# Kernel tuning notes

Hardware: AMD Instinct MI355X
Metric: run time of the kernel (lower is better)

## Reference

```python
import jax, jax.numpy as jnp
import numpy as np

B, N1, N2, E = 128, 128, 384, 1024
N = N1 + N2
D_IN, D_FC = 64, 128
NUM_HEADS = 8.0  # args.num_att_heads
THETA = 1.0      # args.al_scale


def setup_inputs() -> dict:
    key = jax.random.key(0)
    ks = jax.random.split(key, 14)
    c_hs = jax.random.normal(ks[0], (B, N, D_IN), jnp.float32)
    attention = jax.random.uniform(ks[1], (B, N1, N2), jnp.float32)
    coords = jax.random.normal(ks[2], (B, N, 3), jnp.float32)
    upd_coords = coords + 0.1 * jax.random.normal(ks[3], (B, N, 3), jnp.float32)
    c_valid = jnp.ones((B, N), jnp.float32)
    nm = (jax.random.uniform(ks[4], (B, N1)) < 0.7).astype(jnp.float32)
    mapping = (jax.random.uniform(ks[5], (B, N, N)) < 0.05).astype(jnp.float32)
    samelb = jnp.maximum(mapping, (jax.random.uniform(ks[6], (B, N, N)) < 0.1).astype(jnp.float32))
    edge_index = jax.random.randint(ks[7], (B, E, 2), 0, N1, jnp.int32)
    W0 = jax.random.normal(ks[8], (D_IN, D_FC), jnp.float32) * 0.05
    b0 = jnp.zeros((D_FC,), jnp.float32)
    W1 = jax.random.normal(ks[9], (D_FC, D_FC), jnp.float32) * 0.05
    b1 = jnp.zeros((D_FC,), jnp.float32)
    W2 = jax.random.normal(ks[10], (D_FC, D_FC), jnp.float32) * 0.05
    b2 = jnp.zeros((D_FC,), jnp.float32)
    W3 = jax.random.normal(ks[11], (D_FC, 1), jnp.float32) * 0.05
    b3 = jnp.zeros((1,), jnp.float32)
    return dict(c_hs=c_hs, attention=attention, coords=coords, upd_coords=upd_coords,
                c_valid=c_valid, nm=nm, mapping=mapping, samelb=samelb,
                edge_index=edge_index, W0=W0, b0=b0, W1=W1, b1=b1, W2=W2, b2=b2, W3=W3, b3=b3)


def _kabsch(P, Q, m):
    # P, Q: [N1, 3], m: [N1] 0/1 non-modified mask
    Pm = P.mean(0)
    Qm = Q.mean(0)
    h = (P - Pm).T @ (Q - Qm) / NUM_HEADS  # [3,3]
    u, s, vt = jnp.linalg.svd(h)
    d = jnp.sign(jnp.linalg.det(h))
    corr = jnp.diag(jnp.concatenate([jnp.ones((2,), h.dtype), d[None].astype(h.dtype)]))
    r = u @ corr @ vt
    trans = Qm - r @ Pm
    Pp = P @ r.T + trans
    mk = (m > 0.5).astype(P.dtype)[:, None]
    cnt = jnp.maximum(mk.sum() * 3.0, 1.0)
    new_rmsd = (mk * (Pp - Q) ** 2).sum() / cnt        # mse over selected rows
    cen = ((Pp.mean(0) - Qm) ** 2).mean()              # centroid mse
    return new_rmsd, cen


def reference(c_hs, attention, coords, upd_coords, c_valid, nm, mapping, samelb,
              edge_index, W0, b0, W1, b1, W2, b2, W3, b3):
    # --- segment-sum pooling (sum_var_parts) + divide by n1, then FC head ---
    pooled = (c_hs * c_valid[..., None]).sum(axis=1) / float(N1)   # [B, D_IN]
    h = jax.nn.relu(pooled @ W0 + b0)
    h = jax.nn.relu(h @ W1 + b1)
    h = jax.nn.relu(h @ W2 + b2)
    scores = jax.nn.sigmoid(h @ W3 + b3).reshape(-1)               # [B]

    # --- cal_atten_batch + F.normalize(dim=1) ---
    atten = jnp.zeros((B, N, N), c_hs.dtype)
    atten = atten.at[:, :N1, N1:].set(attention)
    atten = atten.at[:, N1:, :N1].set(jnp.swapaxes(attention, 1, 2))
    nrm = jnp.sqrt((atten ** 2).sum(axis=1, keepdims=True))
    atten = atten / jnp.maximum(nrm, 1e-12)

    # --- cal_attn_loss ---
    top = jnp.where(mapping == 1.0, jnp.exp(-(atten * mapping)), 0.0).sum(axis=(1, 2))
    topabot = jnp.where(samelb == 1.0, jnp.exp(-(atten * samelb)), 0.0).sum(axis=(1, 2))
    attn_loss = (top / (topabot - top + 1.0)).sum() * THETA / float(B)

    # --- cal_rmsd_loss: straight-through one-hot mapping + Kabsch/SVD ---
    PP = upd_coords[:, :N1]   # subgraph updated coords
    QQ = coords[:, N1:]       # target graph original coords
    oh = jax.nn.one_hot(jnp.argmax(attention, axis=-1), N2, dtype=attention.dtype)
    st = oh + attention - jax.lax.stop_gradient(attention)         # straight-through
    Qsel = jnp.einsum('bij,bjd->bid', st, QQ)                      # [B, N1, 3]
    new_rmsd, cen = jax.vmap(_kabsch)(PP, Qsel, nm)
    rmsd_loss = new_rmsd.mean()
    centroid_loss = cen.mean()

    # --- cal_pairdst_loss over subgraph edges ---
    sub_c = coords[:, :N1]
    sub_u = upd_coords[:, :N1]
    bidx = jnp.arange(B)[:, None]
    d0 = jnp.sqrt(((sub_c[bidx, edge_index[..., 0]] - sub_c[bidx, edge_index[..., 1]]) ** 2).sum(-1) + 1e-12)
    d1 = jnp.sqrt(((sub_u[bidx, edge_index[..., 0]] - sub_u[bidx, edge_index[..., 1]]) ** 2).sum(-1) + 1e-12)
    pairdst_loss = jnp.abs((d1 - d0).sum(axis=-1)).mean()

    return scores, attn_loss, rmsd_loss, pairdst_loss, centroid_loss
```

## Files before the change

### kernel.cpp

```cpp
#include <hip/hip_runtime.h>
#include <math.h>

#define B_   128
#define N1_  128
#define N2_  384
#define N_   512
#define E_   1024
#define DIN  64
#define DFC  128

#define ACC_TOP  0
#define ACC_BOT  128
#define POOL_OFF 256
#define RNI_OFF  (POOL_OFF + B_*DIN)
#define CNI_OFF  (RNI_OFF + B_*N1_)
#define BI_OFF   (CNI_OFF + B_*N2_)
#define EB_OFF   (BI_OFF + B_*N1_)
#define ZERO_CNT (POOL_OFF + B_*DIN)

__global__ void k_init(float* ws, float* out) {
    int idx = blockIdx.x * 256 + threadIdx.x;
    if (idx < ZERO_CNT) ws[idx] = 0.f;
    if (blockIdx.x == 0 && threadIdx.x < 4) out[128 + threadIdx.x] = 0.f;
}

__global__ void k_pool(const float* __restrict__ c_hs, const float* __restrict__ c_valid,
                       float* __restrict__ ws) {
    __shared__ float4 sred[256];
    int b = blockIdx.x, t = threadIdx.x;
    int chunk = blockIdx.y * 64;
    int d4 = t & 15, rl = t >> 4;
    const float4* X4 = (const float4*)(c_hs + (size_t)b * N_ * DIN);
    const float* V = c_valid + (size_t)b * N_;
    float4 acc = {0.f, 0.f, 0.f, 0.f};
    #pragma unroll
    for (int r = chunk + rl; r < chunk + 64; r += 16) {
        float4 x = X4[r * 16 + d4];
        float v = V[r];
        acc.x += x.x * v; acc.y += x.y * v; acc.z += x.z * v; acc.w += x.w * v;
    }
    sred[t] = acc; __syncthreads();
    for (int off = 128; off >= 16; off >>= 1) {
        if (t < off) {
            float4 o = sred[t + off];
            sred[t].x += o.x; sred[t].y += o.y; sred[t].z += o.z; sred[t].w += o.w;
        }
        __syncthreads();
    }
    if (t < 16) {
        float4 s = sred[t];
        float* p = ws + POOL_OFF + b * DIN + t * 4;
        atomicAdd(&p[0], s.x); atomicAdd(&p[1], s.y);
        atomicAdd(&p[2], s.z); atomicAdd(&p[3], s.w);
    }
}

__global__ void k_mlp2(const float* __restrict__ ws,
                       const float* __restrict__ W0, const float* __restrict__ b0,
                       const float* __restrict__ W1, const float* __restrict__ b1,
                       const float* __restrict__ W2, const float* __restrict__ b2,
                       const float* __restrict__ W3, const float* __restrict__ b3,
                       float* __restrict__ out) {
    __shared__ float pool[DIN];
    __shared__ float h[DFC];
    __shared__ float h2[DFC];
    __shared__ float part[DFC];
    int b = blockIdx.x, t = threadIdx.x;
    if (t < DIN) pool[t] = ws[POOL_OFF + b * DIN + t] * (1.0f / 128.0f);
    __syncthreads();
    float a = b0[t];
    #pragma unroll
    for (int i = 0; i < DIN; ++i) a += pool[i] * W0[i * DFC + t];
    h[t] = fmaxf(a, 0.f); __syncthreads();
    a = b1[t];
    #pragma unroll
    for (int i = 0; i < DFC; ++i) a += h[i] * W1[i * DFC + t];
    h2[t] = fmaxf(a, 0.f); __syncthreads();
    a = b2[t];
    #pragma unroll
    for (int i = 0; i < DFC; ++i) a += h2[i] * W2[i * DFC + t];
    part[t] = fmaxf(a, 0.f) * W3[t];
    __syncthreads();
    for (int off = 64; off > 0; off >>= 1) { if (t < off) part[t] += part[t + off]; __syncthreads(); }
    if (t == 0) out[b] = 1.f / (1.f + expf(-(part[0] + b3[0])));
}

__global__ void k_rows(const float* __restrict__ att, float* __restrict__ ws) {
    int b = blockIdx.x, t = threadIdx.x, wv = t >> 6, ln = t & 63;
    int r = blockIdx.y * 4 + wv;
    const float* row = att + ((size_t)b * N1_ + r) * N2_;
    float ssq = 0.f, best = -1e30f; int bidx = 0;
    #pragma unroll
    for (int q = 0; q < 6; ++q) {
        float v = row[ln + 64 * q];
        ssq += v * v;
        if (v > best) { best = v; bidx = ln + 64 * q; }
    }
    for (int off = 32; off > 0; off >>= 1) {
        ssq += __shfl_xor(ssq, off, 64);
        float ov = __shfl_xor(best, off, 64);
        int oi = __shfl_xor(bidx, off, 64);
        if (ov > best || (ov == best && oi < bidx)) { best = ov; bidx = oi; }
    }
    if (ln == 0) {
        ws[RNI_OFF + b * N1_ + r] = 1.f / fmaxf(sqrtf(ssq), 1e-12f);
        ((int*)ws)[BI_OFF + b * N1_ + r] = bidx;
    }
}

__global__ void k_cols(const float* __restrict__ att, float* __restrict__ ws) {
    __shared__ float sred[256];
    int b = blockIdx.x, t = threadIdx.x;
    int c = blockIdx.y * 64 + (t & 63);
    int q = t >> 6;
    const float* A = att + (size_t)b * N1_ * N2_;
    float s = 0.f;
    #pragma unroll 8
    for (int j = q * 32; j < q * 32 + 32; ++j) { float v = A[j * N2_ + c]; s += v * v; }
    sred[t] = s; __syncthreads();
    if (t < 64)
        ws[CNI_OFF + b * N2_ + blockIdx.y * 64 + t] =
            1.f / fmaxf(sqrtf(sred[t] + sred[t + 64] + sred[t + 128] + sred[t + 192]), 1e-12f);
}

#define TP 129
__global__ void k_prep(const float* __restrict__ att, float* __restrict__ ws) {
    __shared__ float tile[32 * TP];
    __shared__ float rinv[N1_];
    int b = blockIdx.y, t = threadIdx.x;
    int r0 = blockIdx.x * 32;
    if (t < N1_) rinv[t] = ws[RNI_OFF + b * N1_ + t];
    __syncthreads();
    const float4* att4 = (const float4*)(att + (size_t)b * N1_ * N2_);
    int c8 = t & 7, jb = t >> 3;
    #pragma unroll
    for (int p = 0; p < 4; ++p) {
        int j = jb + p * 32;
        float4 a = att4[j * 96 + blockIdx.x * 8 + c8];
        float rv = rinv[j];
        tile[(c8 * 4 + 0) * TP + j] = a.x * rv;
        tile[(c8 * 4 + 1) * TP + j] = a.y * rv;
        tile[(c8 * 4 + 2) * TP + j] = a.z * rv;
        tile[(c8 * 4 + 3) * TP + j] = a.w * rv;
    }
    __syncthreads();
    int j4 = t & 31, cb = t >> 5;
    float4* eb4 = (float4*)(ws + EB_OFF + ((size_t)b * N2_ + r0) * N1_);
    #pragma unroll
    for (int p = 0; p < 4; ++p) {
        int c = cb + p * 8;
        float4 e;
        e.x = __expf(-tile[c * TP + j4 * 4]);
        e.y = __expf(-tile[c * TP + j4 * 4 + 1]);
        e.z = __expf(-tile[c * TP + j4 * 4 + 2]);
        e.w = __expf(-tile[c * TP + j4 * 4 + 3]);
        eb4[c * 32 + j4] = e;
    }
}

__device__ inline float cnt4(float4 m) {
    return (m.x == 1.f ? 1.f : 0.f) + (m.y == 1.f ? 1.f : 0.f)
         + (m.z == 1.f ? 1.f : 0.f) + (m.w == 1.f ? 1.f : 0.f);
}

__global__ void k_scan(const float* __restrict__ att, const float* __restrict__ mapping,
                       const float* __restrict__ samelb, float* __restrict__ ws) {
    __shared__ float cninv[N2_];
    __shared__ float rt[4], rb[4];
    int b = blockIdx.y, t = threadIdx.x;
    int i0 = blockIdx.x * 16;
    const float4* m4 = (const float4*)(mapping + ((size_t)b * N_ + i0) * N_);
    const float4* s4 = (const float4*)(samelb + ((size_t)b * N_ + i0) * N_);
    float top = 0.f, bot = 0.f;
    if (i0 < N1_) {
        for (int j = t; j < N2_; j += 256) cninv[j] = ws[CNI_OFF + b * N2_ + j];
        __syncthreads();
        #pragma unroll
        for (int k = 0; k < 2; ++k) {
            int g = t + k * 256; int r = g >> 5, c4 = g & 31;
            top += cnt4(m4[r * 128 + c4]);
            bot += cnt4(s4[r * 128 + c4]);
        }
        const float4* a4 = (const float4*)(att + ((size_t)b * N1_ + i0) * N2_);
        #pragma unroll
        for (int k = 0; k < 6; ++k) {
            int g = t + k * 256; int r = g / 96, c4 = g - r * 96;
            float4 mv = m4[r * 128 + 32 + c4];
            float4 sv = s4[r * 128 + 32 + c4];
            float4 a  = a4[r * 96 + c4];
            int cb = c4 * 4;
            float e0 = __expf(-a.x * cninv[cb]);
            float e1 = __expf(-a.y * cninv[cb + 1]);
            float e2 = __expf(-a.z * cninv[cb + 2]);
            float e3 = __expf(-a.w * cninv[cb + 3]);
            top += (mv.x == 1.f ? e0 : 0.f) + (mv.y == 1.f ? e1 : 0.f)
                 + (mv.z == 1.f ? e2 : 0.f) + (mv.w == 1.f ? e3 : 0.f);
            bot += (sv.x == 1.f ? e0 : 0.f) + (sv.y == 1.f ? e1 : 0.f)
                 + (sv.z == 1.f ? e2 : 0.f) + (sv.w == 1.f ? e3 : 0.f);
        }
    } else {
        const float4* eb4 = (const float4*)(ws + EB_OFF + ((size_t)b * N2_ + (i0 - N1_)) * N1_);
        #pragma unroll
        for (int k = 0; k < 2; ++k) {
            int g = t + k * 256; int r = g >> 5, c4 = g & 31;
            float4 mv = m4[r * 128 + c4];
            float4 sv = s4[r * 128 + c4];
            float4 e  = eb4[r * 32 + c4];
            top += (mv.x == 1.f ? e.x : 0.f) + (mv.y == 1.f ? e.y : 0.f)
                 + (mv.z == 1.f ? e.z : 0.f) + (mv.w == 1.f ? e.w : 0.f);
            bot += (sv.x == 1.f ? e.x : 0.f) + (sv.y == 1.f ? e.y : 0.f)
                 + (sv.z == 1.f ? e.z : 0.f) + (sv.w == 1.f ? e.w : 0.f);
        }
        #pragma unroll
        for (int k = 0; k < 6; ++k) {
            int g = t + k * 256; int r = g / 96, c4 = g - r * 96;
            top += cnt4(m4[r * 128 + 32 + c4]);
            bot += cnt4(s4[r * 128 + 32 + c4]);
        }
    }
    for (int off = 32; off > 0; off >>= 1) {
        top += __shfl_down(top, off, 64);
        bot += __shfl_down(bot, off, 64);
    }
    int wv = t >> 6, ln = t & 63;
    if (ln == 0) { rt[wv] = top; rb[wv] = bot; }
    __syncthreads();
    if (t == 0) {
        atomicAdd(&ws[ACC_TOP + b], rt[0] + rt[1] + rt[2] + rt[3]);
        atomicAdd(&ws[ACC_BOT + b], rb[0] + rb[1] + rb[2] + rb[3]);
    }
}

__device__ inline float bred(float* s2, float v, int t) {
    for (int off = 32; off > 0; off >>= 1) v += __shfl_down(v, off, 64);
    if ((t & 63) == 0) s2[t >> 6] = v;
    __syncthreads();
    float r = s2[0] + s2[1];
    __syncthreads();
    return r;
}

__global__ void k_kabsch(const float* __restrict__ coords, const float* __restrict__ upd,
                         const float* __restrict__ nm, const int* __restrict__ ei,
                         const float* __restrict__ ws, float* __restrict__ out) {
    __shared__ float s2[2];
    __shared__ float Rsh[9], Tsh[3];
    int b = blockIdx.x, t = threadIdx.x;
    int bidx = ((const int*)ws)[BI_OFF + b * N1_ + t];
    float P[3], Q[3];
    const float* up = upd + ((size_t)b * N_ + t) * 3;
    P[0] = up[0]; P[1] = up[1]; P[2] = up[2];
    const float* qp = coords + ((size_t)b * N_ + N1_ + bidx) * 3;
    Q[0] = qp[0]; Q[1] = qp[1]; Q[2] = qp[2];
    float Pm[3], Qm[3];
    for (int a = 0; a < 3; ++a) Pm[a] = bred(s2, P[a], t) * (1.f / 128.f);
    for (int a = 0; a < 3; ++a) Qm[a] = bred(s2, Q[a], t) * (1.f / 128.f);
    float H[9];
    for (int a = 0; a < 3; ++a)
        for (int c = 0; c < 3; ++c)
            H[a * 3 + c] = bred(s2, (P[a] - Pm[a]) * (Q[c] - Qm[c]), t) * (1.f / 8.f);
    if (t == 0) {
        double Hd[3][3];
        for (int a = 0; a < 3; ++a) for (int c = 0; c < 3; ++c) Hd[a][c] = (double)H[a * 3 + c];
        double A[3][3], V[3][3] = {{1,0,0},{0,1,0},{0,0,1}};
        for (int i = 0; i < 3; ++i)
            for (int j = 0; j < 3; ++j) {
                double z = 0; for (int c = 0; c < 3; ++c) z += Hd[c][i] * Hd[c][j];
                A[i][j] = z;
            }
        for (int sweep = 0; sweep < 8; ++sweep) {
            const int PQ[3][2] = {{0,1},{0,2},{1,2}};
            for (int r = 0; r < 3; ++r) {
                int p = PQ[r][0], q = PQ[r][1];
                double apq = A[p][q];
                if (fabs(apq) < 1e-300) continue;
                double tau = (A[q][q] - A[p][p]) / (2.0 * apq);
                double tt = (tau >= 0 ? 1.0 : -1.0) / (fabs(tau) + sqrt(1.0 + tau * tau));
                double c = 1.0 / sqrt(1.0 + tt * tt), s = tt * c;
                for (int k = 0; k < 3; ++k) { double akp = A[k][p], akq = A[k][q]; A[k][p] = c * akp - s * akq; A[k][q] = s * akp + c * akq; }
                for (int k = 0; k < 3; ++k) { double apk = A[p][k], aqk = A[q][k]; A[p][k] = c * apk - s * aqk; A[q][k] = s * apk + c * aqk; }
                for (int k = 0; k < 3; ++k) { double vkp = V[k][p], vkq = V[k][q]; V[k][p] = c * vkp - s * vkq; V[k][q] = s * vkp + c * vkq; }
            }
        }
        double lam[3] = {A[0][0], A[1][1], A[2][2]};
        int id[3] = {0, 1, 2};
        if (lam[id[0]] < lam[id[1]]) { int x = id[0]; id[0] = id[1]; id[1] = x; }
        if (lam[id[0]] < lam[id[2]]) { int x = id[0]; id[0] = id[2]; id[2] = x; }
        if (lam[id[1]] < lam[id[2]]) { int x = id[1]; id[1] = id[2]; id[2] = x; }
        double u[3][3], v[3][3], sv[3];
        for (int i = 0; i < 3; ++i) {
            for (int k = 0; k < 3; ++k) v[i][k] = V[k][id[i]];
            double uv[3];
            for (int c = 0; c < 3; ++c) uv[c] = Hd[c][0] * v[i][0] + Hd[c][1] * v[i][1] + Hd[c][2] * v[i][2];
            double n = sqrt(uv[0] * uv[0] + uv[1] * uv[1] + uv[2] * uv[2]);
            sv[i] = n;
            if (n > 1e-150) { u[i][0] = uv[0] / n; u[i][1] = uv[1] / n; u[i][2] = uv[2] / n; }
            else { u[i][0] = u[i][1] = u[i][2] = 0.0; }
        }
        if (sv[2] < 1e-12 * fmax(sv[0], 1e-300)) {
            u[2][0] = u[0][1] * u[1][2] - u[0][2] * u[1][1];
            u[2][1] = u[0][2] * u[1][0] - u[0][0] * u[1][2];
            u[2][2] = u[0][0] * u[1][1] - u[0][1] * u[1][0];
        }
        double det = Hd[0][0] * (Hd[1][1] * Hd[2][2] - Hd[1][2] * Hd[2][1])
                   - Hd[0][1] * (Hd[1][0] * Hd[2][2] - Hd[1][2] * Hd[2][0])
                   + Hd[0][2] * (Hd[1][0] * Hd[2][1] - Hd[1][1] * Hd[2][0]);
        double dsg = (det > 0.0) ? 1.0 : ((det < 0.0) ? -1.0 : 0.0);
        for (int a = 0; a < 3; ++a)
            for (int c = 0; c < 3; ++c)
                Rsh[a * 3 + c] = (float)(u[0][a] * v[0][c] + u[1][a] * v[1][c] + dsg * u[2][a] * v[2][c]);
        for (int a = 0; a < 3; ++a)
            Tsh[a] = Qm[a] - (Rsh[a * 3] * Pm[0] + Rsh[a * 3 + 1] * Pm[1] + Rsh[a * 3 + 2] * Pm[2]);
    }
    __syncthreads();
    float Pp[3];
    for (int a = 0; a < 3; ++a)
        Pp[a] = Rsh[a * 3] * P[0] + Rsh[a * 3 + 1] * P[1] + Rsh[a * 3 + 2] * P[2] + Tsh[a];
    float mk = (nm[b * N1_ + t] > 0.5f) ? 1.f : 0.f;
    float dx = Pp[0] - Q[0], dy = Pp[1] - Q[1], dz = Pp[2] - Q[2];
    float rsum = bred(s2, mk * (dx * dx + dy * dy + dz * dz), t);
    float msum = bred(s2, mk, t);
    float Ppm[3];
    for (int a = 0; a < 3; ++a) Ppm[a] = bred(s2, Pp[a], t) * (1.f / 128.f);
    if (t == 0) {
        float cnt = fmaxf(msum * 3.f, 1.f);
        atomicAdd(&out[129], (rsum / cnt) * (1.f / 128.f));
        float cen = 0.f;
        for (int a = 0; a < 3; ++a) { float d2 = Ppm[a] - Qm[a]; cen += d2 * d2; }
        atomicAdd(&out[131], (cen / 3.f) * (1.f / 128.f));
    }
    const float* C = coords + (size_t)b * N_ * 3;
    const float* U = upd + (size_t)b * N_ * 3;
    const int* e = ei + (size_t)b * E_ * 2;
    float acc = 0.f;
    for (int idx = t; idx < E_; idx += 128) {
        int a0 = e[idx * 2], a1 = e[idx * 2 + 1];
        float ex = C[a0 * 3] - C[a1 * 3], ey = C[a0 * 3 + 1] - C[a1 * 3 + 1], ez = C[a0 * 3 + 2] - C[a1 * 3 + 2];
        float d0 = sqrtf(ex * ex + ey * ey + ez * ez + 1e-12f);
        ex = U[a0 * 3] - U[a1 * 3]; ey = U[a0 * 3 + 1] - U[a1 * 3 + 1]; ez = U[a0 * 3 + 2] - U[a1 * 3 + 2];
        float d1 = sqrtf(ex * ex + ey * ey + ez * ez + 1e-12f);
        acc += d1 - d0;
    }
    float psum = bred(s2, acc, t);
    if (t == 0) atomicAdd(&out[130], fabsf(psum) * (1.f / 128.f));
    if (b == 0) {
        float top = ws[ACC_TOP + t], bot = ws[ACC_BOT + t];
        float v = top / (bot - top + 1.0f);
        float s = bred(s2, v, t);
        if (t == 0) out[128] = s * (1.0f / 128.0f);
    }
}

extern "C" void kernel_launch(void* const* d_in, const int* in_sizes, int n_in,
                              void* d_out, int out_size, void* d_ws, size_t ws_size,
                              hipStream_t stream) {
    const float* c_hs      = (const float*)d_in[0];
    const float* attention = (const float*)d_in[1];
    const float* coords    = (const float*)d_in[2];
    const float* upd       = (const float*)d_in[3];
    const float* c_valid   = (const float*)d_in[4];
    const float* nm        = (const float*)d_in[5];
    const float* mapping   = (const float*)d_in[6];
    const float* samelb    = (const float*)d_in[7];
    const int*   ei        = (const int*)d_in[8];
    const float* W0 = (const float*)d_in[9],  *b0 = (const float*)d_in[10];
    const float* W1 = (const float*)d_in[11], *b1 = (const float*)d_in[12];
    const float* W2 = (const float*)d_in[13], *b2 = (const float*)d_in[14];
    const float* W3 = (const float*)d_in[15], *b3 = (const float*)d_in[16];
    float* out = (float*)d_out;
    float* ws  = (float*)d_ws;

    hipLaunchKernelGGL(k_init,   dim3(33),      dim3(256), 0, stream, ws, out);
    hipLaunchKernelGGL(k_pool,   dim3(B_, 8),   dim3(256), 0, stream, c_hs, c_valid, ws);
    hipLaunchKernelGGL(k_mlp2,   dim3(B_),      dim3(DFC), 0, stream, ws,
                       W0, b0, W1, b1, W2, b2, W3, b3, out);
    hipLaunchKernelGGL(k_rows,   dim3(B_, 32),  dim3(256), 0, stream, attention, ws);
    hipLaunchKernelGGL(k_cols,   dim3(B_, 6),   dim3(256), 0, stream, attention, ws);
    hipLaunchKernelGGL(k_prep,   dim3(12, B_),  dim3(256), 0, stream, attention, ws);
    hipLaunchKernelGGL(k_scan,   dim3(32, B_),  dim3(256), 0, stream, attention, mapping, samelb, ws);
    hipLaunchKernelGGL(k_kabsch, dim3(B_),      dim3(N1_), 0, stream, coords, upd, nm, ei, ws, out);
}
```

Before: 389.9 us.

## Precompute attention exponentials and stage scan tiles into LDS via direct global loads

```diff
diff --git a/kernel.cpp b/kernel.cpp
--- a/kernel.cpp
+++ b/kernel.cpp
@@ -16,7 +16,14 @@
 #define CNI_OFF  (RNI_OFF + B_*N1_)
 #define BI_OFF   (CNI_OFF + B_*N2_)
 #define EB_OFF   (BI_OFF + B_*N1_)
+#define EA_OFF   (EB_OFF + B_*N1_*N2_)
 #define ZERO_CNT (POOL_OFF + B_*DIN)
+
+__device__ __forceinline__ void ld_lds16(const float* g, float* l) {
+    __builtin_amdgcn_global_load_lds(
+        (const __attribute__((address_space(1))) void*)g,
+        (__attribute__((address_space(3))) void*)l, 16, 0, 0);
+}
 
 __global__ void k_init(float* ws, float* out) {
     int idx = blockIdx.x * 256 + threadIdx.x;
@@ -123,6 +130,28 @@
             1.f / fmaxf(sqrtf(sred[t] + sred[t + 64] + sred[t + 128] + sred[t + 192]), 1e-12f);
 }
 
+__global__ void k_prepA(const float* __restrict__ att, float* __restrict__ ws) {
+    __shared__ float cni[N2_];
+    int b = blockIdx.x, t = threadIdx.x;
+    int r0 = blockIdx.y * 16;
+    for (int j = t; j < N2_; j += 256) cni[j] = ws[CNI_OFF + b * N2_ + j];
+    __syncthreads();
+    const float4* a4 = (const float4*)(att + ((size_t)b * N1_ + r0) * N2_);
+    float4* e4 = (float4*)(ws + EA_OFF + ((size_t)b * N1_ + r0) * N2_);
+    #pragma unroll
+    for (int k = 0; k < 6; ++k) {
+        int idx = t + k * 256;
+        int c4 = idx % 96; int cb = c4 * 4;
+        float4 a = a4[idx];
+        float4 e;
+        e.x = __expf(-a.x * cni[cb]);
+        e.y = __expf(-a.y * cni[cb + 1]);
+        e.z = __expf(-a.z * cni[cb + 2]);
+        e.w = __expf(-a.w * cni[cb + 3]);
+        e4[idx] = e;
+    }
+}
+
 #define TP 129
 __global__ void k_prep(const float* __restrict__ att, float* __restrict__ ws) {
     __shared__ float tile[32 * TP];
@@ -158,71 +187,59 @@
     }
 }
 
-__device__ inline float cnt4(float4 m) {
-    return (m.x == 1.f ? 1.f : 0.f) + (m.y == 1.f ? 1.f : 0.f)
-         + (m.z == 1.f ? 1.f : 0.f) + (m.w == 1.f ? 1.f : 0.f);
-}
-
-__global__ void k_scan(const float* __restrict__ att, const float* __restrict__ mapping,
-                       const float* __restrict__ samelb, float* __restrict__ ws) {
-    __shared__ float cninv[N2_];
+__global__ void k_scan(const float* __restrict__ mapping, const float* __restrict__ samelb,
+                       float* __restrict__ ws) {
+    __shared__ float4 lm4[512];
+    __shared__ float4 ls4[512];
+    __shared__ float4 le4[384];
     __shared__ float rt[4], rb[4];
     int b = blockIdx.y, t = threadIdx.x;
-    int i0 = blockIdx.x * 16;
-    const float4* m4 = (const float4*)(mapping + ((size_t)b * N_ + i0) * N_);
-    const float4* s4 = (const float4*)(samelb + ((size_t)b * N_ + i0) * N_);
+    int i0 = blockIdx.x * 4;
+    int wv = t >> 6, ln = t & 63;
+    float* lm = (float*)lm4;
+    float* lsm = (float*)ls4;
+    const float* gm = mapping + ((size_t)b * N_ + i0) * N_;
+    const float* gs = samelb + ((size_t)b * N_ + i0) * N_;
+    for (int g = wv; g < 8; g += 4) ld_lds16(gm + g * 256 + ln * 4, lm + g * 256);
+    for (int g = wv; g < 8; g += 4) ld_lds16(gs + g * 256 + ln * 4, lsm + g * 256);
+    bool typeA = (i0 < N1_);
+    if (typeA) {
+        const float* ge = ws + EA_OFF + ((size_t)b * N1_ + i0) * N2_;
+        for (int g = wv; g < 6; g += 4) ld_lds16(ge + g * 256 + ln * 4, (float*)le4 + g * 256);
+    } else {
+        const float* ge = ws + EB_OFF + ((size_t)b * N2_ + (i0 - N1_)) * N1_;
+        for (int g = wv; g < 2; g += 4) ld_lds16(ge + g * 256 + ln * 4, (float*)le4 + g * 256);
+    }
+    __syncthreads();
+    const float4 ONES = {1.f, 1.f, 1.f, 1.f};
     float top = 0.f, bot = 0.f;
-    if (i0 < N1_) {
-        for (int j = t; j < N2_; j += 256) cninv[j] = ws[CNI_OFF + b * N2_ + j];
-        __syncthreads();
+    if (typeA) {
         #pragma unroll
         for (int k = 0; k < 2; ++k) {
-            int g = t + k * 256; int r = g >> 5, c4 = g & 31;
-            top += cnt4(m4[r * 128 + c4]);
-            bot += cnt4(s4[r * 128 + c4]);
-        }
-        const float4* a4 = (const float4*)(att + ((size_t)b * N1_ + i0) * N2_);
-        #pragma unroll
-        for (int k = 0; k < 6; ++k) {
-            int g = t + k * 256; int r = g / 96, c4 = g - r * 96;
-            float4 mv = m4[r * 128 + 32 + c4];
-            float4 sv = s4[r * 128 + 32 + c4];
-            float4 a  = a4[r * 96 + c4];
-            int cb = c4 * 4;
-            float e0 = __expf(-a.x * cninv[cb]);
-            float e1 = __expf(-a.y * cninv[cb + 1]);
-            float e2 = __expf(-a.z * cninv[cb + 2]);
-            float e3 = __expf(-a.w * cninv[cb + 3]);
-            top += (mv.x == 1.f ? e0 : 0.f) + (mv.y == 1.f ? e1 : 0.f)
-                 + (mv.z == 1.f ? e2 : 0.f) + (mv.w == 1.f ? e3 : 0.f);
-            bot += (sv.x == 1.f ? e0 : 0.f) + (sv.y == 1.f ? e1 : 0.f)
-                 + (sv.z == 1.f ? e2 : 0.f) + (sv.w == 1.f ? e3 : 0.f);
+            int idx = t + k * 256;
+            int row = idx >> 7, c4 = idx & 127;
+            float4 m = lm4[idx], s = ls4[idx];
+            int ei = row * 96 + ((c4 < 32) ? 0 : (c4 - 32));
+            float4 w = (c4 < 32) ? ONES : le4[ei];
+            top += m.x * w.x + m.y * w.y + m.z * w.z + m.w * w.w;
+            bot += s.x * w.x + s.y * w.y + s.z * w.z + s.w * w.w;
         }
     } else {
-        const float4* eb4 = (const float4*)(ws + EB_OFF + ((size_t)b * N2_ + (i0 - N1_)) * N1_);
         #pragma unroll
         for (int k = 0; k < 2; ++k) {
-            int g = t + k * 256; int r = g >> 5, c4 = g & 31;
-            float4 mv = m4[r * 128 + c4];
-            float4 sv = s4[r * 128 + c4];
-            float4 e  = eb4[r * 32 + c4];
-            top += (mv.x == 1.f ? e.x : 0.f) + (mv.y == 1.f ? e.y : 0.f)
-                 + (mv.z == 1.f ? e.z : 0.f) + (mv.w == 1.f ? e.w : 0.f);
-            bot += (sv.x == 1.f ? e.x : 0.f) + (sv.y == 1.f ? e.y : 0.f)
-                 + (sv.z == 1.f ? e.z : 0.f) + (sv.w == 1.f ? e.w : 0.f);
-        }
-        #pragma unroll
-        for (int k = 0; k < 6; ++k) {
-            int g = t + k * 256; int r = g / 96, c4 = g - r * 96;
-            top += cnt4(m4[r * 128 + 32 + c4]);
-            bot += cnt4(s4[r * 128 + 32 + c4]);
+            int idx = t + k * 256;
+            int row = idx >> 7, c4 = idx & 127;
+            float4 m = lm4[idx], s = ls4[idx];
+            int ei = row * 32 + ((c4 < 32) ? c4 : 0);
+            float4 w = (c4 < 32) ? le4[ei] : ONES;
+            top += m.x * w.x + m.y * w.y + m.z * w.z + m.w * w.w;
+            bot += s.x * w.x + s.y * w.y + s.z * w.z + s.w * w.w;
         }
     }
     for (int off = 32; off > 0; off >>= 1) {
         top += __shfl_down(top, off, 64);
         bot += __shfl_down(bot, off, 64);
     }
-    int wv = t >> 6, ln = t & 63;
     if (ln == 0) { rt[wv] = top; rb[wv] = bot; }
     __syncthreads();
     if (t == 0) {
@@ -376,7 +393,8 @@
                        W0, b0, W1, b1, W2, b2, W3, b3, out);
     hipLaunchKernelGGL(k_rows,   dim3(B_, 32),  dim3(256), 0, stream, attention, ws);
     hipLaunchKernelGGL(k_cols,   dim3(B_, 6),   dim3(256), 0, stream, attention, ws);
+    hipLaunchKernelGGL(k_prepA,  dim3(B_, 8),   dim3(256), 0, stream, attention, ws);
     hipLaunchKernelGGL(k_prep,   dim3(12, B_),  dim3(256), 0, stream, attention, ws);
-    hipLaunchKernelGGL(k_scan,   dim3(32, B_),  dim3(256), 0, stream, attention, mapping, samelb, ws);
+    hipLaunchKernelGGL(k_scan,   dim3(128, B_), dim3(256), 0, stream, mapping, samelb, ws);
     hipLaunchKernelGGL(k_kabsch, dim3(B_),      dim3(N1_), 0, stream, coords, upd, nm, ei, ws, out);
 }
```

New measurement: 410.1 us. 1.05x slower.

## Merge front-end kernels, fold MLP into Kabsch launch, and simplify scan to two rows per block

Applied to the files above, without the earlier changes.

```diff
diff --git a/kernel.cpp b/kernel.cpp
--- a/kernel.cpp
+++ b/kernel.cpp
@@ -24,103 +24,70 @@
     if (blockIdx.x == 0 && threadIdx.x < 4) out[128 + threadIdx.x] = 0.f;
 }
 
-__global__ void k_pool(const float* __restrict__ c_hs, const float* __restrict__ c_valid,
-                       float* __restrict__ ws) {
-    __shared__ float4 sred[256];
-    int b = blockIdx.x, t = threadIdx.x;
-    int chunk = blockIdx.y * 64;
-    int d4 = t & 15, rl = t >> 4;
-    const float4* X4 = (const float4*)(c_hs + (size_t)b * N_ * DIN);
-    const float* V = c_valid + (size_t)b * N_;
-    float4 acc = {0.f, 0.f, 0.f, 0.f};
-    #pragma unroll
-    for (int r = chunk + rl; r < chunk + 64; r += 16) {
-        float4 x = X4[r * 16 + d4];
-        float v = V[r];
-        acc.x += x.x * v; acc.y += x.y * v; acc.z += x.z * v; acc.w += x.w * v;
-    }
-    sred[t] = acc; __syncthreads();
-    for (int off = 128; off >= 16; off >>= 1) {
-        if (t < off) {
-            float4 o = sred[t + off];
-            sred[t].x += o.x; sred[t].y += o.y; sred[t].z += o.z; sred[t].w += o.w;
-        }
-        __syncthreads();
-    }
-    if (t < 16) {
-        float4 s = sred[t];
-        float* p = ws + POOL_OFF + b * DIN + t * 4;
-        atomicAdd(&p[0], s.x); atomicAdd(&p[1], s.y);
-        atomicAdd(&p[2], s.z); atomicAdd(&p[3], s.w);
-    }
-}
-
-__global__ void k_mlp2(const float* __restrict__ ws,
-                       const float* __restrict__ W0, const float* __restrict__ b0,
-                       const float* __restrict__ W1, const float* __restrict__ b1,
-                       const float* __restrict__ W2, const float* __restrict__ b2,
-                       const float* __restrict__ W3, const float* __restrict__ b3,
-                       float* __restrict__ out) {
-    __shared__ float pool[DIN];
-    __shared__ float h[DFC];
-    __shared__ float h2[DFC];
-    __shared__ float part[DFC];
-    int b = blockIdx.x, t = threadIdx.x;
-    if (t < DIN) pool[t] = ws[POOL_OFF + b * DIN + t] * (1.0f / 128.0f);
-    __syncthreads();
-    float a = b0[t];
-    #pragma unroll
-    for (int i = 0; i < DIN; ++i) a += pool[i] * W0[i * DFC + t];
-    h[t] = fmaxf(a, 0.f); __syncthreads();
-    a = b1[t];
-    #pragma unroll
-    for (int i = 0; i < DFC; ++i) a += h[i] * W1[i * DFC + t];
-    h2[t] = fmaxf(a, 0.f); __syncthreads();
-    a = b2[t];
-    #pragma unroll
-    for (int i = 0; i < DFC; ++i) a += h2[i] * W2[i * DFC + t];
-    part[t] = fmaxf(a, 0.f) * W3[t];
-    __syncthreads();
-    for (int off = 64; off > 0; off >>= 1) { if (t < off) part[t] += part[t + off]; __syncthreads(); }
-    if (t == 0) out[b] = 1.f / (1.f + expf(-(part[0] + b3[0])));
-}
-
-__global__ void k_rows(const float* __restrict__ att, float* __restrict__ ws) {
-    int b = blockIdx.x, t = threadIdx.x, wv = t >> 6, ln = t & 63;
-    int r = blockIdx.y * 4 + wv;
-    const float* row = att + ((size_t)b * N1_ + r) * N2_;
-    float ssq = 0.f, best = -1e30f; int bidx = 0;
-    #pragma unroll
-    for (int q = 0; q < 6; ++q) {
-        float v = row[ln + 64 * q];
-        ssq += v * v;
-        if (v > best) { best = v; bidx = ln + 64 * q; }
-    }
-    for (int off = 32; off > 0; off >>= 1) {
-        ssq += __shfl_xor(ssq, off, 64);
-        float ov = __shfl_xor(best, off, 64);
-        int oi = __shfl_xor(bidx, off, 64);
-        if (ov > best || (ov == best && oi < bidx)) { best = ov; bidx = oi; }
-    }
-    if (ln == 0) {
-        ws[RNI_OFF + b * N1_ + r] = 1.f / fmaxf(sqrtf(ssq), 1e-12f);
-        ((int*)ws)[BI_OFF + b * N1_ + r] = bidx;
-    }
-}
-
-__global__ void k_cols(const float* __restrict__ att, float* __restrict__ ws) {
-    __shared__ float sred[256];
-    int b = blockIdx.x, t = threadIdx.x;
-    int c = blockIdx.y * 64 + (t & 63);
-    int q = t >> 6;
-    const float* A = att + (size_t)b * N1_ * N2_;
-    float s = 0.f;
-    #pragma unroll 8
-    for (int j = q * 32; j < q * 32 + 32; ++j) { float v = A[j * N2_ + c]; s += v * v; }
-    sred[t] = s; __syncthreads();
-    if (t < 64)
-        ws[CNI_OFF + b * N2_ + blockIdx.y * 64 + t] =
-            1.f / fmaxf(sqrtf(sred[t] + sred[t + 64] + sred[t + 128] + sred[t + 192]), 1e-12f);
+__global__ void k_front(const float* __restrict__ c_hs, const float* __restrict__ c_valid,
+                        const float* __restrict__ att, float* __restrict__ ws) {
+    __shared__ float4 sred4[256];
+    float* sred = (float*)sred4;
+    int b = blockIdx.x, y = blockIdx.y, t = threadIdx.x;
+    if (y < 8) {
+        int chunk = y * 64;
+        int d4 = t & 15, rl = t >> 4;
+        const float4* X4 = (const float4*)(c_hs + (size_t)b * N_ * DIN);
+        const float* V = c_valid + (size_t)b * N_;
+        float4 acc = {0.f, 0.f, 0.f, 0.f};
+        #pragma unroll
+        for (int r = chunk + rl; r < chunk + 64; r += 16) {
+            float4 x = X4[r * 16 + d4];
+            float v = V[r];
+            acc.x += x.x * v; acc.y += x.y * v; acc.z += x.z * v; acc.w += x.w * v;
+        }
+        sred4[t] = acc; __syncthreads();
+        for (int off = 128; off >= 16; off >>= 1) {
+            if (t < off) {
+                float4 o = sred4[t + off];
+                sred4[t].x += o.x; sred4[t].y += o.y; sred4[t].z += o.z; sred4[t].w += o.w;
+            }
+            __syncthreads();
+        }
+        if (t < 16) {
+            float4 s = sred4[t];
+            float* p = ws + POOL_OFF + b * DIN + t * 4;
+            atomicAdd(&p[0], s.x); atomicAdd(&p[1], s.y);
+            atomicAdd(&p[2], s.z); atomicAdd(&p[3], s.w);
+        }
+    } else if (y < 40) {
+        int wv = t >> 6, ln = t & 63;
+        int r = (y - 8) * 4 + wv;
+        const float* row = att + ((size_t)b * N1_ + r) * N2_;
+        float ssq = 0.f, best = -1e30f; int bidx = 0;
+        #pragma unroll
+        for (int q = 0; q < 6; ++q) {
+            float v = row[ln + 64 * q];
+            ssq += v * v;
+            if (v > best) { best = v; bidx = ln + 64 * q; }
+        }
+        for (int off = 32; off > 0; off >>= 1) {
+            ssq += __shfl_xor(ssq, off, 64);
+            float ov = __shfl_xor(best, off, 64);
+            int oi = __shfl_xor(bidx, off, 64);
+            if (ov > best || (ov == best && oi < bidx)) { best = ov; bidx = oi; }
+        }
+        if (ln == 0) {
+            ws[RNI_OFF + b * N1_ + r] = 1.f / fmaxf(sqrtf(ssq), 1e-12f);
+            ((int*)ws)[BI_OFF + b * N1_ + r] = bidx;
+        }
+    } else {
+        int c = (y - 40) * 64 + (t & 63);
+        int q = t >> 6;
+        const float* A = att + (size_t)b * N1_ * N2_;
+        float s = 0.f;
+        #pragma unroll 8
+        for (int j = q * 32; j < q * 32 + 32; ++j) { float v = A[j * N2_ + c]; s += v * v; }
+        sred[t] = s; __syncthreads();
+        if (t < 64)
+            ws[CNI_OFF + b * N2_ + (y - 40) * 64 + t] =
+                1.f / fmaxf(sqrtf(sred[t] + sred[t + 64] + sred[t + 128] + sred[t + 192]), 1e-12f);
+    }
 }
 
 #define TP 129
@@ -158,66 +125,34 @@
     }
 }
 
-__device__ inline float cnt4(float4 m) {
-    return (m.x == 1.f ? 1.f : 0.f) + (m.y == 1.f ? 1.f : 0.f)
-         + (m.z == 1.f ? 1.f : 0.f) + (m.w == 1.f ? 1.f : 0.f);
-}
-
 __global__ void k_scan(const float* __restrict__ att, const float* __restrict__ mapping,
                        const float* __restrict__ samelb, float* __restrict__ ws) {
-    __shared__ float cninv[N2_];
     __shared__ float rt[4], rb[4];
     int b = blockIdx.y, t = threadIdx.x;
-    int i0 = blockIdx.x * 16;
-    const float4* m4 = (const float4*)(mapping + ((size_t)b * N_ + i0) * N_);
-    const float4* s4 = (const float4*)(samelb + ((size_t)b * N_ + i0) * N_);
-    float top = 0.f, bot = 0.f;
-    if (i0 < N1_) {
-        for (int j = t; j < N2_; j += 256) cninv[j] = ws[CNI_OFF + b * N2_ + j];
-        __syncthreads();
-        #pragma unroll
-        for (int k = 0; k < 2; ++k) {
-            int g = t + k * 256; int r = g >> 5, c4 = g & 31;
-            top += cnt4(m4[r * 128 + c4]);
-            bot += cnt4(s4[r * 128 + c4]);
-        }
-        const float4* a4 = (const float4*)(att + ((size_t)b * N1_ + i0) * N2_);
-        #pragma unroll
-        for (int k = 0; k < 6; ++k) {
-            int g = t + k * 256; int r = g / 96, c4 = g - r * 96;
-            float4 mv = m4[r * 128 + 32 + c4];
-            float4 sv = s4[r * 128 + 32 + c4];
-            float4 a  = a4[r * 96 + c4];
-            int cb = c4 * 4;
-            float e0 = __expf(-a.x * cninv[cb]);
-            float e1 = __expf(-a.y * cninv[cb + 1]);
-            float e2 = __expf(-a.z * cninv[cb + 2]);
-            float e3 = __expf(-a.w * cninv[cb + 3]);
-            top += (mv.x == 1.f ? e0 : 0.f) + (mv.y == 1.f ? e1 : 0.f)
-                 + (mv.z == 1.f ? e2 : 0.f) + (mv.w == 1.f ? e3 : 0.f);
-            bot += (sv.x == 1.f ? e0 : 0.f) + (sv.y == 1.f ? e1 : 0.f)
-                 + (sv.z == 1.f ? e2 : 0.f) + (sv.w == 1.f ? e3 : 0.f);
+    int i = 2 * blockIdx.x + (t >> 7);
+    int c4 = t & 127;
+    const float4* m4 = (const float4*)(mapping + ((size_t)b * N_ + i) * N_);
+    const float4* s4 = (const float4*)(samelb + ((size_t)b * N_ + i) * N_);
+    float4 m = m4[c4];
+    float4 s = s4[c4];
+    float4 w = {1.f, 1.f, 1.f, 1.f};
+    if (i < N1_) {
+        if (c4 >= 32) {
+            int a4i = c4 - 32;
+            float4 a = ((const float4*)(att + ((size_t)b * N1_ + i) * N2_))[a4i];
+            float4 cn = ((const float4*)(ws + CNI_OFF + b * N2_))[a4i];
+            w.x = __expf(-a.x * cn.x);
+            w.y = __expf(-a.y * cn.y);
+            w.z = __expf(-a.z * cn.z);
+            w.w = __expf(-a.w * cn.w);
         }
     } else {
-        const float4* eb4 = (const float4*)(ws + EB_OFF + ((size_t)b * N2_ + (i0 - N1_)) * N1_);
-        #pragma unroll
-        for (int k = 0; k < 2; ++k) {
-            int g = t + k * 256; int r = g >> 5, c4 = g & 31;
-            float4 mv = m4[r * 128 + c4];
-            float4 sv = s4[r * 128 + c4];
-            float4 e  = eb4[r * 32 + c4];
-            top += (mv.x == 1.f ? e.x : 0.f) + (mv.y == 1.f ? e.y : 0.f)
-                 + (mv.z == 1.f ? e.z : 0.f) + (mv.w == 1.f ? e.w : 0.f);
-            bot += (sv.x == 1.f ? e.x : 0.f) + (sv.y == 1.f ? e.y : 0.f)
-                 + (sv.z == 1.f ? e.z : 0.f) + (sv.w == 1.f ? e.w : 0.f);
-        }
-        #pragma unroll
-        for (int k = 0; k < 6; ++k) {
-            int g = t + k * 256; int r = g / 96, c4 = g - r * 96;
-            top += cnt4(m4[r * 128 + 32 + c4]);
-            bot += cnt4(s4[r * 128 + 32 + c4]);
-        }
-    }
+        if (c4 < 32) {
+            w = ((const float4*)(ws + EB_OFF + ((size_t)b * N2_ + (i - N1_)) * N1_))[c4];
+        }
+    }
+    float top = m.x * w.x + m.y * w.y + m.z * w.z + m.w * w.w;
+    float bot = s.x * w.x + s.y * w.y + s.z * w.z + s.w * w.w;
     for (int off = 32; off > 0; off >>= 1) {
         top += __shfl_down(top, off, 64);
         bot += __shfl_down(bot, off, 64);
@@ -240,12 +175,42 @@
     return r;
 }
 
-__global__ void k_kabsch(const float* __restrict__ coords, const float* __restrict__ upd,
-                         const float* __restrict__ nm, const int* __restrict__ ei,
-                         const float* __restrict__ ws, float* __restrict__ out) {
-    __shared__ float s2[2];
+__global__ void k_back(const float* __restrict__ coords, const float* __restrict__ upd,
+                       const float* __restrict__ nm, const int* __restrict__ ei,
+                       const float* __restrict__ W0, const float* __restrict__ b0,
+                       const float* __restrict__ W1, const float* __restrict__ b1,
+                       const float* __restrict__ W2, const float* __restrict__ b2,
+                       const float* __restrict__ W3, const float* __restrict__ b3,
+                       const float* __restrict__ ws, float* __restrict__ out) {
+    __shared__ float sh[2 * DFC];
+    int b = blockIdx.x, t = threadIdx.x;
+    if (blockIdx.y == 1) {
+        float* pool = sh;
+        float* h    = sh + 64;
+        __shared__ float part[DFC];
+        if (t < DIN) pool[t] = ws[POOL_OFF + b * DIN + t] * (1.0f / 128.0f);
+        __syncthreads();
+        float a = b0[t];
+        #pragma unroll
+        for (int i = 0; i < DIN; ++i) a += pool[i] * W0[i * DFC + t];
+        float hv = fmaxf(a, 0.f);
+        __syncthreads(); h[t] = hv; __syncthreads();
+        a = b1[t];
+        #pragma unroll
+        for (int i = 0; i < DFC; ++i) a += h[i] * W1[i * DFC + t];
+        hv = fmaxf(a, 0.f);
+        __syncthreads(); h[t] = hv; __syncthreads();
+        a = b2[t];
+        #pragma unroll
+        for (int i = 0; i < DFC; ++i) a += h[i] * W2[i * DFC + t];
+        part[t] = fmaxf(a, 0.f) * W3[t];
+        __syncthreads();
+        for (int off = 64; off > 0; off >>= 1) { if (t < off) part[t] += part[t + off]; __syncthreads(); }
+        if (t == 0) out[b] = 1.f / (1.f + expf(-(part[0] + b3[0])));
+        return;
+    }
+    float* s2 = sh;
     __shared__ float Rsh[9], Tsh[3];
-    int b = blockIdx.x, t = threadIdx.x;
     int bidx = ((const int*)ws)[BI_OFF + b * N1_ + t];
     float P[3], Q[3];
     const float* up = upd + ((size_t)b * N_ + t) * 3;
@@ -370,13 +335,10 @@
     float* out = (float*)d_out;
     float* ws  = (float*)d_ws;
 
-    hipLaunchKernelGGL(k_init,   dim3(33),      dim3(256), 0, stream, ws, out);
-    hipLaunchKernelGGL(k_pool,   dim3(B_, 8),   dim3(256), 0, stream, c_hs, c_valid, ws);
-    hipLaunchKernelGGL(k_mlp2,   dim3(B_),      dim3(DFC), 0, stream, ws,
-                       W0, b0, W1, b1, W2, b2, W3, b3, out);
-    hipLaunchKernelGGL(k_rows,   dim3(B_, 32),  dim3(256), 0, stream, attention, ws);
-    hipLaunchKernelGGL(k_cols,   dim3(B_, 6),   dim3(256), 0, stream, attention, ws);
-    hipLaunchKernelGGL(k_prep,   dim3(12, B_),  dim3(256), 0, stream, attention, ws);
-    hipLaunchKernelGGL(k_scan,   dim3(32, B_),  dim3(256), 0, stream, attention, mapping, samelb, ws);
-    hipLaunchKernelGGL(k_kabsch, dim3(B_),      dim3(N1_), 0, stream, coords, upd, nm, ei, ws, out);
-}
+    hipLaunchKernelGGL(k_init,  dim3(33),       dim3(256), 0, stream, ws, out);
+    hipLaunchKernelGGL(k_front, dim3(B_, 46),   dim3(256), 0, stream, c_hs, c_valid, attention, ws);
+    hipLaunchKernelGGL(k_prep,  dim3(12, B_),   dim3(256), 0, stream, attention, ws);
+    hipLaunchKernelGGL(k_scan,  dim3(256, B_),  dim3(256), 0, stream, attention, mapping, samelb, ws);
+    hipLaunchKernelGGL(k_back,  dim3(B_, 2),    dim3(128), 0, stream, coords, upd, nm, ei,
+                       W0, b0, W1, b1, W2, b2, W3, b3, ws, out);
+}
```

Result: slower. 479.1 us (+22.9%).
